# Optimization experiments

Hardware: AMD Instinct MI355X
Metric: run time of the kernel (lower is better)

The kernel has to match this reference:

```python
import jax, jax.numpy as jnp
import numpy as np

N_ATOMS = 32768
N_SPECIES = 4
N_FEAT = 7584
HIDDEN = 256
N_STRUCT = 1024


def setup_inputs() -> dict:
    key = jax.random.key(0)
    ks = jax.random.split(key, 12)
    s = 1.0 / np.sqrt(N_FEAT)
    h = 1.0 / np.sqrt(HIDDEN)
    return {
        "features": jax.random.normal(ks[0], (N_ATOMS, N_FEAT), dtype=jnp.float32),
        "structure_index": jax.random.randint(ks[1], (N_ATOMS,), 0, N_STRUCT),
        "n_structures": N_STRUCT,
        "W1": jax.random.normal(ks[2], (N_SPECIES, N_FEAT, HIDDEN), dtype=jnp.float32) * s,
        "b1": jax.random.normal(ks[3], (N_SPECIES, HIDDEN), dtype=jnp.float32) * s,
        "W2": jax.random.normal(ks[4], (N_SPECIES, HIDDEN, HIDDEN), dtype=jnp.float32) * h,
        "b2": jax.random.normal(ks[5], (N_SPECIES, HIDDEN), dtype=jnp.float32) * h,
        "W3": jax.random.normal(ks[6], (N_SPECIES, HIDDEN, HIDDEN), dtype=jnp.float32) * h,
        "b3": jax.random.normal(ks[7], (N_SPECIES, HIDDEN), dtype=jnp.float32) * h,
        "W4": jax.random.normal(ks[8], (N_SPECIES, HIDDEN), dtype=jnp.float32) * h,
        "b4": jax.random.normal(ks[9], (N_SPECIES,), dtype=jnp.float32) * h,
    }


def reference(features, structure_index, n_structures, W1, b1, W2, b2, W3, b3, W4, b4):
    # Atoms are stored as contiguous per-species blocks (as in the equistore
    # TensorMap), so the species-gated gather is a reshape: [S, A, F].
    S = W1.shape[0]
    x = features.reshape(S, -1, features.shape[-1])
    # Per-species 4-layer MLP (grouped GEMMs).
    hdn = jax.nn.silu(jnp.einsum("saf,sfh->sah", x, W1) + b1[:, None, :])
    hdn = jax.nn.silu(jnp.einsum("sah,shk->sak", hdn, W2) + b2[:, None, :])
    hdn = jax.nn.silu(jnp.einsum("sah,shk->sak", hdn, W3) + b3[:, None, :])
    atomic_energies = (jnp.einsum("sah,sh->sa", hdn, W4) + b4[:, None]).reshape(-1)
    # Scatter-add atomic energies into per-structure energies (index_add_).
    energies = jax.ops.segment_sum(atomic_energies, structure_index,
                                   num_segments=n_structures)
    return energies
```

## Files before the change

kernel.cpp:

```cpp
#include <hip/hip_runtime.h>
#include <hip/hip_bf16.h>

#define N_ATOMS   32768
#define N_SPECIES 4
#define N_FEAT    7584
#define HIDDEN    256
#define N_STRUCT  1024
#define APS       8192

typedef __attribute__((ext_vector_type(8))) short bf16x8;
typedef __attribute__((ext_vector_type(4))) float f32x4;

typedef const __attribute__((address_space(1))) void* gptr_t;
typedef __attribute__((address_space(3))) void* lptr_t;

__device__ __forceinline__ unsigned short f2bf(float x) {
    union { float f; unsigned u; } v; v.f = x;
    unsigned r = v.u + 0x7FFFu + ((v.u >> 16) & 1u);
    return (unsigned short)(r >> 16);
}
__device__ __forceinline__ float bf2f(unsigned short h) {
    union { unsigned u; float f; } v; v.u = ((unsigned)h) << 16;
    return v.f;
}

__global__ void transpose_cvt(const float* __restrict__ in,
                              unsigned short* __restrict__ out,
                              int K, int N) {
    __shared__ unsigned short sh[32][33];
    const int s  = blockIdx.z;
    const int k0 = blockIdx.x * 32;
    const int n0 = blockIdx.y * 32;
    const int tx = threadIdx.x & 31;
    const int ty = threadIdx.x >> 5;
    const float* ip = in + (size_t)s * K * N;
    unsigned short* op = out + (size_t)s * N * K;
#pragma unroll
    for (int i = 0; i < 4; ++i) {
        int k = ty + 8 * i;
        sh[tx][k] = f2bf(ip[(size_t)(k0 + k) * N + n0 + tx]);
    }
    __syncthreads();
#pragma unroll
    for (int i = 0; i < 4; ++i) {
        int n = ty + 8 * i;
        op[(size_t)(n0 + n) * K + k0 + tx] = sh[n][tx];
    }
}


__device__ __forceinline__ void stage_B(const unsigned short* __restrict__ Wts,
                                        int K, int k0,
                                        unsigned short* BsmBuf, int w, int lane) {
#pragma unroll
    for (int j = 0; j < 4; ++j) {
        const unsigned short* gp =
            Wts + (size_t)(16 * (4 * w + j) + (lane >> 2)) * K + k0 + (lane & 3) * 8;
        __builtin_amdgcn_global_load_lds((gptr_t)gp,
                                         (lptr_t)&BsmBuf[(4 * w + j) * 512],
                                         16, 0, 0);
    }
}

__device__ __forceinline__ void load_A(const float* __restrict__ Af, int K, int k0,
                                       int tid, float4 v[2]) {
#pragma unroll
    for (int r = 0; r < 2; ++r) {
        int f = tid + 256 * r;
        int row = f >> 3, c4 = f & 7;
        v[r] = *(const float4*)(Af + (size_t)row * K + k0 + c4 * 4);
    }
}
__device__ __forceinline__ void commit_A(unsigned short* AsmBuf, int tid,
                                         const float4 v[2]) {
#pragma unroll
    for (int r = 0; r < 2; ++r) {
        int f = tid + 256 * r;
        int row = f >> 3, c4 = f & 7;
        ushort4 b;
        b.x = f2bf(v[r].x); b.y = f2bf(v[r].y);
        b.z = f2bf(v[r].z); b.w = f2bf(v[r].w);
        *(ushort4*)(&AsmBuf[row * 48 + c4 * 4]) = b;
    }
}

#define HPAD 264

__global__ __launch_bounds__(256, 2) void fused_mlp(
    const float* __restrict__ features,
    const unsigned short* __restrict__ Wt1,
    const float* __restrict__ b1,
    const unsigned short* __restrict__ Wt2,
    const float* __restrict__ b2,
    const unsigned short* __restrict__ Wt3,
    const float* __restrict__ b3,
    const float* __restrict__ W4,
    const float* __restrict__ b4,
    const int* __restrict__ sidx,
    float* __restrict__ out) {
    __shared__ unsigned short Asm[2][64 * 48];
    __shared__ unsigned short Bsm[2][256 * 32];
    __shared__ unsigned short Hsm[64 * HPAD];

    const int tid  = threadIdx.x;
    const int w    = tid >> 6;
    const int lane = tid & 63;
    const int lm   = lane & 15;
    const int q    = lane >> 4;
    const int kgl  = q * 8;
    const int s    = blockIdx.x >> 7;
    const int m0   = (blockIdx.x & 127) * 64;

    f32x4 acc[4][4];

    {
        const float* Af = features + ((size_t)s * APS + m0) * N_FEAT;
        const unsigned short* Wts = Wt1 + (size_t)s * 256 * N_FEAT;
#pragma unroll
        for (int i = 0; i < 4; ++i)
#pragma unroll
            for (int j = 0; j < 4; ++j)
#pragma unroll
                for (int e = 0; e < 4; ++e) acc[i][j][e] = 0.0f;

        float4 av[2];
        stage_B(Wts, N_FEAT, 0, Bsm[0], w, lane);
        load_A(Af, N_FEAT, 0, tid, av);
        commit_A(Asm[0], tid, av);

        int buf = 0;
        for (int k0 = 0; k0 < N_FEAT; k0 += 32, buf ^= 1) {
            __syncthreads();
            const bool more = (k0 + 32 < N_FEAT);
            if (more) {
                stage_B(Wts, N_FEAT, k0 + 32, Bsm[buf ^ 1], w, lane);
                load_A(Af, N_FEAT, k0 + 32, tid, av);
            }
            bf16x8 af[4], bfr[4];
#pragma unroll
            for (int mf = 0; mf < 4; ++mf)
                af[mf] = *(const bf16x8*)(&Asm[buf][(mf * 16 + lm) * 48 + kgl]);
#pragma unroll
            for (int nf = 0; nf < 4; ++nf)
                bfr[nf] = *(const bf16x8*)(&Bsm[buf][(w * 64 + nf * 16 + lm) * 32 + kgl]);
#pragma unroll
            for (int mf = 0; mf < 4; ++mf)
#pragma unroll
                for (int nf = 0; nf < 4; ++nf)
                    acc[mf][nf] = __builtin_amdgcn_mfma_f32_16x16x32_bf16(
                        af[mf], bfr[nf], acc[mf][nf], 0, 0, 0);
            if (more) commit_A(Asm[buf ^ 1], tid, av);
        }
        __syncthreads();
        const float* bp = b1 + s * 256;
#pragma unroll
        for (int nf = 0; nf < 4; ++nf) {
            int col = w * 64 + nf * 16 + lm;
            float bv = bp[col];
#pragma unroll
            for (int mf = 0; mf < 4; ++mf)
#pragma unroll
                for (int i = 0; i < 4; ++i) {
                    int row = mf * 16 + q * 4 + i;
                    float x = acc[mf][nf][i] + bv;
                    Hsm[row * HPAD + col] = f2bf(x / (1.0f + __expf(-x)));
                }
        }
    }

#pragma unroll 1
    for (int layer = 0; layer < 2; ++layer) {
        const unsigned short* Wts =
            (layer == 0 ? Wt2 : Wt3) + (size_t)s * 256 * 256;
        const float* bp = (layer == 0 ? b2 : b3) + s * 256;
#pragma unroll
        for (int i = 0; i < 4; ++i)
#pragma unroll
            for (int j = 0; j < 4; ++j)
#pragma unroll
                for (int e = 0; e < 4; ++e) acc[i][j][e] = 0.0f;

        stage_B(Wts, 256, 0, Bsm[0], w, lane);
        int buf = 0;
        for (int k0 = 0; k0 < 256; k0 += 32, buf ^= 1) {
            __syncthreads();
            if (k0 + 32 < 256)
                stage_B(Wts, 256, k0 + 32, Bsm[buf ^ 1], w, lane);
            bf16x8 af[4], bfr[4];
#pragma unroll
            for (int mf = 0; mf < 4; ++mf)
                af[mf] = *(const bf16x8*)(&Hsm[(mf * 16 + lm) * HPAD + k0 + kgl]);
#pragma unroll
            for (int nf = 0; nf < 4; ++nf)
                bfr[nf] = *(const bf16x8*)(&Bsm[buf][(w * 64 + nf * 16 + lm) * 32 + kgl]);
#pragma unroll
            for (int mf = 0; mf < 4; ++mf)
#pragma unroll
                for (int nf = 0; nf < 4; ++nf)
                    acc[mf][nf] = __builtin_amdgcn_mfma_f32_16x16x32_bf16(
                        af[mf], bfr[nf], acc[mf][nf], 0, 0, 0);
        }
        __syncthreads();
#pragma unroll
        for (int nf = 0; nf < 4; ++nf) {
            int col = w * 64 + nf * 16 + lm;
            float bv = bp[col];
#pragma unroll
            for (int mf = 0; mf < 4; ++mf)
#pragma unroll
                for (int i = 0; i < 4; ++i) {
                    int row = mf * 16 + q * 4 + i;
                    float x = acc[mf][nf][i] + bv;
                    Hsm[row * HPAD + col] = f2bf(x / (1.0f + __expf(-x)));
                }
        }
    }

    __syncthreads();
    {
        const float* W4s = W4 + s * 256;
        const int a_loc = w * 16 + lm;
        float sum = 0.0f;
#pragma unroll
        for (int j8 = 0; j8 < 8; ++j8) {
            bf16x8 hv = *(const bf16x8*)(&Hsm[a_loc * HPAD + q * 64 + j8 * 8]);
            float4 w0 = *(const float4*)(W4s + q * 64 + j8 * 8);
            float4 w1 = *(const float4*)(W4s + q * 64 + j8 * 8 + 4);
            sum += bf2f((unsigned short)hv[0]) * w0.x + bf2f((unsigned short)hv[1]) * w0.y +
                   bf2f((unsigned short)hv[2]) * w0.z + bf2f((unsigned short)hv[3]) * w0.w +
                   bf2f((unsigned short)hv[4]) * w1.x + bf2f((unsigned short)hv[5]) * w1.y +
                   bf2f((unsigned short)hv[6]) * w1.z + bf2f((unsigned short)hv[7]) * w1.w;
        }
        sum += __shfl_xor(sum, 16, 64);
        sum += __shfl_xor(sum, 32, 64);
        if (q == 0) {
            int atom = s * APS + m0 + a_loc;
            atomicAdd(&out[sidx[atom]], sum + b4[s]);
        }
    }
}

extern "C" void kernel_launch(void* const* d_in, const int* in_sizes, int n_in,
                              void* d_out, int out_size, void* d_ws, size_t ws_size,
                              hipStream_t stream) {
    const float* features = (const float*)d_in[0];
    const int*   sidx     = (const int*)d_in[1];
    const float* W1 = (const float*)d_in[3];
    const float* b1 = (const float*)d_in[4];
    const float* W2 = (const float*)d_in[5];
    const float* b2 = (const float*)d_in[6];
    const float* W3 = (const float*)d_in[7];
    const float* b3 = (const float*)d_in[8];
    const float* W4 = (const float*)d_in[9];
    const float* b4 = (const float*)d_in[10];
    float* out = (float*)d_out;

    char* ws = (char*)d_ws;
    unsigned short* Wt1 = (unsigned short*)ws; ws += (size_t)N_SPECIES * HIDDEN * N_FEAT * 2;
    unsigned short* Wt2 = (unsigned short*)ws; ws += (size_t)N_SPECIES * HIDDEN * HIDDEN * 2;
    unsigned short* Wt3 = (unsigned short*)ws; ws += (size_t)N_SPECIES * HIDDEN * HIDDEN * 2;

    hipMemsetAsync(d_out, 0, N_STRUCT * sizeof(float), stream);

    transpose_cvt<<<dim3(N_FEAT / 32, HIDDEN / 32, N_SPECIES), 256, 0, stream>>>(W1, Wt1, N_FEAT, HIDDEN);
    transpose_cvt<<<dim3(HIDDEN / 32, HIDDEN / 32, N_SPECIES), 256, 0, stream>>>(W2, Wt2, HIDDEN, HIDDEN);
    transpose_cvt<<<dim3(HIDDEN / 32, HIDDEN / 32, N_SPECIES), 256, 0, stream>>>(W3, Wt3, HIDDEN, HIDDEN);

    fused_mlp<<<dim3(N_ATOMS / 64), 256, 0, stream>>>(
        features, Wt1, b1, Wt2, b2, Wt3, b3, W4, b4, sidx, out);
}
```

Before: 1.442 ms.

## Split fused MLP into layer-1 GEMM kernel and tail kernel via workspace

Splits the fused MLP kernel into two. The first kernel runs the large layer-1 GEMM without the hidden-activation shared buffer, with launch bounds raised to 3 blocks per CU, and interleaves block IDs so neighbouring blocks share a species' weights. It writes the bf16 activations to a workspace buffer, and the second kernel runs layers 2-4 plus the scatter-add. The aim is more occupancy and better weight cache reuse for the dominant GEMM, at the cost of an extra round trip of about 16MB through global memory and an extra launch. The fused path is kept as a fallback when the workspace is too small.

```diff
diff --git a/kernel.cpp b/kernel.cpp
--- a/kernel.cpp
+++ b/kernel.cpp
@@ -48,7 +48,6 @@
     }
 }
 
-
 __device__ __forceinline__ void stage_B(const unsigned short* __restrict__ Wts,
                                         int K, int k0,
                                         unsigned short* BsmBuf, int w, int lane) {
@@ -85,6 +84,189 @@
 }
 
 #define HPAD 264
+
+__global__ __launch_bounds__(256, 3) void layer1_gemm(
+    const float* __restrict__ features,
+    const unsigned short* __restrict__ Wt1,
+    const float* __restrict__ b1,
+    unsigned short* __restrict__ H) {
+    __shared__ unsigned short Asm[2][64 * 48];
+    __shared__ unsigned short Bsm[2][256 * 32];
+
+    const int tid  = threadIdx.x;
+    const int w    = tid >> 6;
+    const int lane = tid & 63;
+    const int lm   = lane & 15;
+    const int q    = lane >> 4;
+    const int kgl  = q * 8;
+
+    const int bid = blockIdx.x;
+    const int s   = (bid & 7) >> 1;
+    const int m0  = (((bid >> 3) << 1) | (bid & 1)) * 64;
+
+    const float* Af = features + ((size_t)s * APS + m0) * N_FEAT;
+    const unsigned short* Wts = Wt1 + (size_t)s * 256 * N_FEAT;
+
+    f32x4 acc[4][4];
+#pragma unroll
+    for (int i = 0; i < 4; ++i)
+#pragma unroll
+        for (int j = 0; j < 4; ++j)
+#pragma unroll
+            for (int e = 0; e < 4; ++e) acc[i][j][e] = 0.0f;
+
+    float4 av[2];
+    stage_B(Wts, N_FEAT, 0, Bsm[0], w, lane);
+    load_A(Af, N_FEAT, 0, tid, av);
+    commit_A(Asm[0], tid, av);
+
+    int buf = 0;
+    for (int k0 = 0; k0 < N_FEAT; k0 += 32, buf ^= 1) {
+        __syncthreads();
+        const bool more = (k0 + 32 < N_FEAT);
+        if (more) {
+            stage_B(Wts, N_FEAT, k0 + 32, Bsm[buf ^ 1], w, lane);
+            load_A(Af, N_FEAT, k0 + 32, tid, av);
+        }
+        bf16x8 af[4], bfr[4];
+#pragma unroll
+        for (int mf = 0; mf < 4; ++mf)
+            af[mf] = *(const bf16x8*)(&Asm[buf][(mf * 16 + lm) * 48 + kgl]);
+#pragma unroll
+        for (int nf = 0; nf < 4; ++nf)
+            bfr[nf] = *(const bf16x8*)(&Bsm[buf][(w * 64 + nf * 16 + lm) * 32 + kgl]);
+#pragma unroll
+        for (int mf = 0; mf < 4; ++mf)
+#pragma unroll
+            for (int nf = 0; nf < 4; ++nf)
+                acc[mf][nf] = __builtin_amdgcn_mfma_f32_16x16x32_bf16(
+                    af[mf], bfr[nf], acc[mf][nf], 0, 0, 0);
+        if (more) commit_A(Asm[buf ^ 1], tid, av);
+    }
+
+    const float* bp = b1 + s * 256;
+    unsigned short* Hp = H + ((size_t)s * APS + m0) * 256;
+#pragma unroll
+    for (int nf = 0; nf < 4; ++nf) {
+        int col = w * 64 + nf * 16 + lm;
+        float bv = bp[col];
+#pragma unroll
+        for (int mf = 0; mf < 4; ++mf)
+#pragma unroll
+            for (int i = 0; i < 4; ++i) {
+                int row = mf * 16 + q * 4 + i;
+                float x = acc[mf][nf][i] + bv;
+                Hp[(size_t)row * 256 + col] = f2bf(x / (1.0f + __expf(-x)));
+            }
+    }
+}
+
+__global__ __launch_bounds__(256, 2) void mlp_tail(
+    const unsigned short* __restrict__ H,
+    const unsigned short* __restrict__ Wt2,
+    const float* __restrict__ b2,
+    const unsigned short* __restrict__ Wt3,
+    const float* __restrict__ b3,
+    const float* __restrict__ W4,
+    const float* __restrict__ b4,
+    const int* __restrict__ sidx,
+    float* __restrict__ out) {
+    __shared__ unsigned short Hsm[64 * HPAD];
+    __shared__ unsigned short Bsm[2][256 * 32];
+
+    const int tid  = threadIdx.x;
+    const int w    = tid >> 6;
+    const int lane = tid & 63;
+    const int lm   = lane & 15;
+    const int q    = lane >> 4;
+    const int kgl  = q * 8;
+    const int s    = blockIdx.x >> 7;
+    const int m0   = (blockIdx.x & 127) * 64;
+
+    {
+        const unsigned short* Hg = H + ((size_t)s * APS + m0) * 256;
+#pragma unroll
+        for (int i = 0; i < 8; ++i) {
+            int c = tid + (i << 8);
+            int row = c >> 5, chunk = c & 31;
+            bf16x8 v = *(const bf16x8*)(Hg + (size_t)row * 256 + chunk * 8);
+            *(bf16x8*)(&Hsm[row * HPAD + chunk * 8]) = v;
+        }
+    }
+
+    f32x4 acc[4][4];
+
+#pragma unroll 1
+    for (int layer = 0; layer < 2; ++layer) {
+        const unsigned short* Wts =
+            (layer == 0 ? Wt2 : Wt3) + (size_t)s * 256 * 256;
+        const float* bp = (layer == 0 ? b2 : b3) + s * 256;
+#pragma unroll
+        for (int i = 0; i < 4; ++i)
+#pragma unroll
+            for (int j = 0; j < 4; ++j)
+#pragma unroll
+                for (int e = 0; e < 4; ++e) acc[i][j][e] = 0.0f;
+
+        stage_B(Wts, 256, 0, Bsm[0], w, lane);
+        int buf = 0;
+        for (int k0 = 0; k0 < 256; k0 += 32, buf ^= 1) {
+            __syncthreads();
+            if (k0 + 32 < 256)
+                stage_B(Wts, 256, k0 + 32, Bsm[buf ^ 1], w, lane);
+            bf16x8 af[4], bfr[4];
+#pragma unroll
+            for (int mf = 0; mf < 4; ++mf)
+                af[mf] = *(const bf16x8*)(&Hsm[(mf * 16 + lm) * HPAD + k0 + kgl]);
+#pragma unroll
+            for (int nf = 0; nf < 4; ++nf)
+                bfr[nf] = *(const bf16x8*)(&Bsm[buf][(w * 64 + nf * 16 + lm) * 32 + kgl]);
+#pragma unroll
+            for (int mf = 0; mf < 4; ++mf)
+#pragma unroll
+                for (int nf = 0; nf < 4; ++nf)
+                    acc[mf][nf] = __builtin_amdgcn_mfma_f32_16x16x32_bf16(
+                        af[mf], bfr[nf], acc[mf][nf], 0, 0, 0);
+        }
+        __syncthreads();
+#pragma unroll
+        for (int nf = 0; nf < 4; ++nf) {
+            int col = w * 64 + nf * 16 + lm;
+            float bv = bp[col];
+#pragma unroll
+            for (int mf = 0; mf < 4; ++mf)
+#pragma unroll
+                for (int i = 0; i < 4; ++i) {
+                    int row = mf * 16 + q * 4 + i;
+                    float x = acc[mf][nf][i] + bv;
+                    Hsm[row * HPAD + col] = f2bf(x / (1.0f + __expf(-x)));
+                }
+        }
+    }
+
+    __syncthreads();
+    {
+        const float* W4s = W4 + s * 256;
+        const int a_loc = w * 16 + lm;
+        float sum = 0.0f;
+#pragma unroll
+        for (int j8 = 0; j8 < 8; ++j8) {
+            bf16x8 hv = *(const bf16x8*)(&Hsm[a_loc * HPAD + q * 64 + j8 * 8]);
+            float4 w0 = *(const float4*)(W4s + q * 64 + j8 * 8);
+            float4 w1 = *(const float4*)(W4s + q * 64 + j8 * 8 + 4);
+            sum += bf2f((unsigned short)hv[0]) * w0.x + bf2f((unsigned short)hv[1]) * w0.y +
+                   bf2f((unsigned short)hv[2]) * w0.z + bf2f((unsigned short)hv[3]) * w0.w +
+                   bf2f((unsigned short)hv[4]) * w1.x + bf2f((unsigned short)hv[5]) * w1.y +
+                   bf2f((unsigned short)hv[6]) * w1.z + bf2f((unsigned short)hv[7]) * w1.w;
+        }
+        sum += __shfl_xor(sum, 16, 64);
+        sum += __shfl_xor(sum, 32, 64);
+        if (q == 0) {
+            int atom = s * APS + m0 + a_loc;
+            atomicAdd(&out[sidx[atom]], sum + b4[s]);
+        }
+    }
+}
 
 __global__ __launch_bounds__(256, 2) void fused_mlp(
     const float* __restrict__ features,
@@ -255,10 +437,16 @@
     const float* b4 = (const float*)d_in[10];
     float* out = (float*)d_out;
 
+    const size_t wt1_b = (size_t)N_SPECIES * HIDDEN * N_FEAT * 2;
+    const size_t wt2_b = (size_t)N_SPECIES * HIDDEN * HIDDEN * 2;
+    const size_t hb_b  = (size_t)N_ATOMS * HIDDEN * 2;
+    const size_t need_split = wt1_b + 2 * wt2_b + hb_b;
+
     char* ws = (char*)d_ws;
-    unsigned short* Wt1 = (unsigned short*)ws; ws += (size_t)N_SPECIES * HIDDEN * N_FEAT * 2;
-    unsigned short* Wt2 = (unsigned short*)ws; ws += (size_t)N_SPECIES * HIDDEN * HIDDEN * 2;
-    unsigned short* Wt3 = (unsigned short*)ws; ws += (size_t)N_SPECIES * HIDDEN * HIDDEN * 2;
+    unsigned short* Wt1 = (unsigned short*)ws; ws += wt1_b;
+    unsigned short* Wt2 = (unsigned short*)ws; ws += wt2_b;
+    unsigned short* Wt3 = (unsigned short*)ws; ws += wt2_b;
+    unsigned short* Hb  = (unsigned short*)ws; ws += hb_b;
 
     hipMemsetAsync(d_out, 0, N_STRUCT * sizeof(float), stream);
 
@@ -266,6 +454,12 @@
     transpose_cvt<<<dim3(HIDDEN / 32, HIDDEN / 32, N_SPECIES), 256, 0, stream>>>(W2, Wt2, HIDDEN, HIDDEN);
     transpose_cvt<<<dim3(HIDDEN / 32, HIDDEN / 32, N_SPECIES), 256, 0, stream>>>(W3, Wt3, HIDDEN, HIDDEN);
 
-    fused_mlp<<<dim3(N_ATOMS / 64), 256, 0, stream>>>(
-        features, Wt1, b1, Wt2, b2, Wt3, b3, W4, b4, sidx, out);
-}
+    if (ws_size >= need_split) {
+        layer1_gemm<<<dim3(N_ATOMS / 64), 256, 0, stream>>>(features, Wt1, b1, Hb);
+        mlp_tail<<<dim3(N_ATOMS / 64), 256, 0, stream>>>(
+            Hb, Wt2, b2, Wt3, b3, W4, b4, sidx, out);
+    } else {
+        fused_mlp<<<dim3(N_ATOMS / 64), 256, 0, stream>>>(
+            features, Wt1, b1, Wt2, b2, Wt3, b3, W4, b4, sidx, out);
+    }
+}
```

Result: no change. 1.447 ms (+0.4%).
